# Optimization experiments

Measured on AMD Instinct MI355X. Metric: run time of the kernel, lower is better.

## Reference

```python
import jax, jax.numpy as jnp
import numpy as np

N_EMBD = 2048
N_HEAD = 32
N_KV_HEADS = 8
HEAD_DIM = 64
N_REP = N_HEAD // N_KV_HEADS
MAX_SEQ_LEN = 4096
ROPE_THETA = 10000.0


def _precompute_freqs_cis(dim, end, theta=ROPE_THETA):
    freqs = 1.0 / theta ** (jnp.arange(0, dim, 2)[: dim // 2].astype(jnp.float32) / dim)
    t = jnp.arange(end, dtype=jnp.float32)
    freqs = jnp.outer(t, freqs)  # (end, dim//2)
    return jnp.cos(freqs), jnp.sin(freqs)


def setup_inputs() -> dict:
    key = jax.random.key(0)
    ks = jax.random.split(key, 5)
    B, S = 2, 2048
    x = jax.random.normal(ks[0], (B, S, N_EMBD), dtype=jnp.float32)
    # torch Linear(in, out, bias=False): y = x @ W.T, W is (out, in). We store (in, out).
    sc = 1.0 / np.sqrt(N_EMBD)
    wq = jax.random.normal(ks[1], (N_EMBD, N_EMBD), dtype=jnp.float32) * sc
    wk = jax.random.normal(ks[2], (N_EMBD, N_KV_HEADS * HEAD_DIM), dtype=jnp.float32) * sc
    wv = jax.random.normal(ks[3], (N_EMBD, N_KV_HEADS * HEAD_DIM), dtype=jnp.float32) * sc
    wo = jax.random.normal(ks[4], (N_EMBD, N_EMBD), dtype=jnp.float32) * sc
    freqs_cos, freqs_sin = _precompute_freqs_cis(HEAD_DIM, MAX_SEQ_LEN)
    return {"x": x, "wq": wq, "wk": wk, "wv": wv, "wo": wo,
            "freqs_cos": freqs_cos, "freqs_sin": freqs_sin}


def _apply_rotary(t, cos, sin):
    # t: (B, S, H, HD); interleaved real/imag pairs along last dim.
    shp = t.shape
    t2 = t.reshape(*shp[:-1], HEAD_DIM // 2, 2)
    r, i = t2[..., 0], t2[..., 1]
    out_r = r * cos - i * sin
    out_i = r * sin + i * cos
    return jnp.stack([out_r, out_i], axis=-1).reshape(shp)


def reference(x, wq, wk, wv, wo, freqs_cos, freqs_sin):
    B, S, _ = x.shape
    xq = (x @ wq).reshape(B, S, N_HEAD, HEAD_DIM)
    xk = (x @ wk).reshape(B, S, N_KV_HEADS, HEAD_DIM)
    xv = (x @ wv).reshape(B, S, N_KV_HEADS, HEAD_DIM)

    cos = freqs_cos[:S][None, :, None, :]  # (1, S, 1, HD/2)
    sin = freqs_sin[:S][None, :, None, :]
    xq = _apply_rotary(xq, cos, sin)
    xk = _apply_rotary(xk, cos, sin)

    # GQA: repeat KV heads (repeat_interleave along head dim)
    keys = jnp.repeat(xk, N_REP, axis=2)    # (B, S, H, HD)
    values = jnp.repeat(xv, N_REP, axis=2)

    scores = jnp.einsum('bqhd,bkhd->bhqk', xq, keys) / np.sqrt(HEAD_DIM)
    causal = jnp.tril(jnp.ones((S, S), dtype=bool))
    scores = jnp.where(causal, scores, -jnp.inf)
    probs = jax.nn.softmax(scores.astype(jnp.float32), axis=-1).astype(xq.dtype)
    out = jnp.einsum('bhqk,bkhd->bqhd', probs, values)  # (B, S, H, HD)
    out = out.reshape(B, S, N_EMBD)
    return out @ wo
```

## Files before the change

kernel.cpp:

```cpp
#include <hip/hip_runtime.h>
#include <hip/hip_fp16.h>
#include <stdint.h>

typedef _Float16 f16x8 __attribute__((ext_vector_type(8)));
typedef _Float16 f16x4 __attribute__((ext_vector_type(4)));
typedef _Float16 f16x2 __attribute__((ext_vector_type(2)));
typedef float f32x4 __attribute__((ext_vector_type(4)));
typedef float f32x16 __attribute__((ext_vector_type(16)));

#define B_ 2
#define S_ 2048
#define NE 2048
#define NH 32
#define NKV 8
#define HD 64
#define NTOK (B_ * S_)
#define QKVN 3072

__device__ __forceinline__ f16x2 pk(float a, float b) {
  return __builtin_bit_cast(f16x2, __builtin_amdgcn_cvt_pkrtz(a, b));
}

__device__ __forceinline__ void gld_lds16(void* lds, const void* g) {
  __builtin_amdgcn_global_load_lds(
      (const __attribute__((address_space(1))) void*)g,
      (__attribute__((address_space(3))) void*)lds, 16, 0, 0);
}

#define PREP_CONV 16384
__global__ __launch_bounds__(256) void prep_kernel(
    const float* __restrict__ x, _Float16* __restrict__ xb,
    const float* __restrict__ wq, const float* __restrict__ wk,
    const float* __restrict__ wv, const float* __restrict__ wo,
    _Float16* __restrict__ wqkv_t, _Float16* __restrict__ wo_t) {
  const int bid = blockIdx.x;
  const int tid = threadIdx.x;
  if (bid < PREP_CONV) {
    int i = bid * 256 + tid;
    float2 v = ((const float2*)x)[i];
    f16x2 h;
    h.x = (_Float16)v.x;
    h.y = (_Float16)v.y;
    ((f16x2*)xb)[i] = h;
    return;
  }
  __shared__ float tile[32][33];
  int r = bid - PREP_CONV;
  const float* src;
  _Float16* dst;
  int srcN, rowoff, bx, by;
  if (r < 4096) {
    src = wq; dst = wqkv_t; srcN = 2048; rowoff = 0;
    bx = r & 63; by = r >> 6;
  } else if (r < 5120) {
    r -= 4096;
    src = wk; dst = wqkv_t; srcN = 512; rowoff = 2048;
    bx = r & 15; by = r >> 4;
  } else if (r < 6144) {
    r -= 5120;
    src = wv; dst = wqkv_t; srcN = 512; rowoff = 2560;
    bx = r & 15; by = r >> 4;
  } else {
    r -= 6144;
    src = wo; dst = wo_t; srcN = 2048; rowoff = 0;
    bx = r & 63; by = r >> 6;
  }
  const int n0 = bx * 32, k0 = by * 32;
  const int tx = tid & 31, ty = tid >> 5;
  for (int i = ty; i < 32; i += 8)
    tile[i][tx] = src[(size_t)(k0 + i) * srcN + n0 + tx];
  __syncthreads();
  for (int i = ty; i < 32; i += 8)
    dst[(size_t)(rowoff + n0 + i) * 2048 + k0 + tx] = (_Float16)tile[tx][i];
}

template <int OUT_F32>
__global__ __launch_bounds__(256, 2) void gemm_bt(
    const _Float16* __restrict__ A, const _Float16* __restrict__ Bt,
    void* __restrict__ Cout, int M, int N, int K) {
  __shared__ _Float16 As[128 * 32];
  __shared__ _Float16 Bs[128 * 32];
  const int tid = threadIdx.x;
  const int wave = tid >> 6, lane = tid & 63;
  const int qd = lane >> 4, ln = lane & 15;
  const int m0 = blockIdx.y * 128, n0 = blockIdx.x * 128;
  const int wm = (wave >> 1) * 64, wn = (wave & 1) * 64;

  f32x4 acc[4][4] = {};

  const int srow = (lane >> 2);
  const int scol = (lane & 3) * 8;

  for (int k0 = 0; k0 < K; k0 += 32) {
    __syncthreads();
#pragma unroll
    for (int it = 0; it < 2; ++it) {
      int r = wave * 32 + it * 16 + srow;
      gld_lds16(&As[(wave * 32 + it * 16) * 32],
                A + (size_t)(m0 + r) * K + k0 + scol);
      gld_lds16(&Bs[(wave * 32 + it * 16) * 32],
                Bt + (size_t)(n0 + r) * K + k0 + scol);
    }
    __syncthreads();
    f16x8 a[4], b[4];
#pragma unroll
    for (int mt = 0; mt < 4; ++mt)
      a[mt] = *(const f16x8*)&As[(wm + mt * 16 + ln) * 32 + qd * 8];
#pragma unroll
    for (int nt = 0; nt < 4; ++nt)
      b[nt] = *(const f16x8*)&Bs[(wn + nt * 16 + ln) * 32 + qd * 8];
#pragma unroll
    for (int mt = 0; mt < 4; ++mt)
#pragma unroll
      for (int nt = 0; nt < 4; ++nt)
        acc[mt][nt] =
            __builtin_amdgcn_mfma_f32_16x16x32_f16(a[mt], b[nt], acc[mt][nt], 0, 0, 0);
  }

#pragma unroll
  for (int mt = 0; mt < 4; ++mt) {
    int row = m0 + wm + mt * 16 + qd * 4;
#pragma unroll
    for (int nt = 0; nt < 4; ++nt) {
      int col = n0 + wn + nt * 16 + ln;
#pragma unroll
      for (int r = 0; r < 4; ++r) {
        if (OUT_F32)
          ((float*)Cout)[(size_t)(row + r) * N + col] = acc[mt][nt][r];
        else
          ((_Float16*)Cout)[(size_t)(row + r) * N + col] =
              (_Float16)acc[mt][nt][r];
      }
    }
  }
}

#define ROPE_BLKS 20480
__global__ __launch_bounds__(256) void rope_vtrans_kernel(
    const _Float16* __restrict__ qkv, const float* __restrict__ fcos,
    const float* __restrict__ fsin, _Float16* __restrict__ Qb,
    _Float16* __restrict__ Kb, _Float16* __restrict__ Vtg) {
  const int tid = threadIdx.x;
  if (blockIdx.x < ROPE_BLKS) {
    const float QSC = 0.125f * 1.44269504088896f;
    int idx = blockIdx.x * 256 + tid;
    int t = idx / 1280;
    int col = (idx - t * 1280) * 2;
    int b = t >> 11, s = t & 2047;
    float v0 = (float)qkv[(size_t)t * QKVN + col];
    float v1 = (float)qkv[(size_t)t * QKVN + col + 1];
    _Float16* dst;
    size_t off;
    int d;
    float sc;
    if (col < 2048) {
      int h = col >> 6;
      d = col & 63;
      dst = Qb;
      off = ((size_t)(b * NH + h) * S_ + s) * HD + d;
      sc = QSC;
    } else {
      int cc = col - 2048;
      int h = cc >> 6;
      d = cc & 63;
      dst = Kb;
      off = ((size_t)(b * NKV + h) * S_ + s) * HD + d;
      sc = 1.0f;
    }
    float c = fcos[s * 32 + (d >> 1)], sn = fsin[s * 32 + (d >> 1)];
    f16x2 o;
    o.x = (_Float16)((v0 * c - v1 * sn) * sc);
    o.y = (_Float16)((v0 * sn + v1 * c) * sc);
    *(f16x2*)(dst + off) = o;
    return;
  }
  __shared__ _Float16 tile[64][65];
  int r = blockIdx.x - ROPE_BLKS;
  int t0 = (r & 31) * 64;
  int kv = (r >> 5) & 7, b = r >> 8;
  for (int slot = tid; slot < 4096; slot += 256) {
    int rr = slot >> 6, c = slot & 63;
    tile[rr][c] = qkv[(size_t)(b * S_ + t0 + rr) * QKVN + 2560 + kv * 64 + c];
  }
  __syncthreads();
  size_t base = ((size_t)(b * NKV + kv) * HD) * S_;
  for (int slot = tid; slot < 4096; slot += 256) {
    int d = slot >> 6, rr = slot & 63;
    Vtg[base + (size_t)d * S_ + t0 + rr] = tile[rr][d];
  }
}

__global__ __launch_bounds__(128, 2) void attn_kernel(
    const _Float16* __restrict__ Qb, const _Float16* __restrict__ Kb,
    const _Float16* __restrict__ Vtg, _Float16* __restrict__ Ob) {
  constexpr float M_SHIFT = 10.0f;
  __shared__ _Float16 Ks[64 * 64];
  __shared__ _Float16 Vs[64 * 64];
  const int tid = threadIdx.x;
  const int wave = tid >> 6, lane = tid & 63;
  const int mrow = lane & 31;
  const bool half = (lane >> 5) != 0;
  const int h = blockIdx.y, b = blockIdx.z;
  const int kvh = h >> 2;

  const _Float16* Qh = Qb + ((size_t)(b * NH + h) * S_) * HD;
  const _Float16* Kh = Kb + ((size_t)(b * NKV + kvh) * S_) * HD;
  const _Float16* Vh = Vtg + ((size_t)(b * NKV + kvh) * HD) * S_;

  const int sr = tid >> 3;
  const int scc = tid & 7;
  const int swz = (scc ^ (sr & 7)) * 8;

#pragma unroll
  for (int pass = 0; pass < 2; ++pass) {
    const int qt = pass ? blockIdx.x : (31 - blockIdx.x);
    const int q0 = qt * 64;
    const int nkt = qt + 1;

    const int qrow = q0 + wave * 32 + mrow;
    f16x8 aq[4];
#pragma unroll
    for (int kk = 0; kk < 4; ++kk)
      aq[kk] = *(const f16x8*)(Qh + (size_t)qrow * HD + kk * 16 +
                               (half ? 8 : 0));

    f32x16 accO[2] = {};
    float lsum = 0.f;

    f16x8 kp[4], vp[4];
#pragma unroll
    for (int i = 0; i < 4; ++i) {
      kp[i] = *(const f16x8*)(Kh + (size_t)(sr + i * 16) * HD + scc * 8);
      vp[i] = *(const f16x8*)(Vh + (size_t)(sr + i * 16) * S_ + scc * 8);
    }
#pragma unroll
    for (int i = 0; i < 4; ++i) {
      *(f16x8*)&Ks[(sr + i * 16) * 64 + swz] = kp[i];
      *(f16x8*)&Vs[(sr + i * 16) * 64 + swz] = vp[i];
    }

    for (int kt = 0; kt < nkt; ++kt) {
      __syncthreads();
      if (kt + 1 < nkt) {
#pragma unroll
        for (int i = 0; i < 4; ++i) {
          kp[i] = *(const f16x8*)(Kh +
                                  (size_t)((kt + 1) * 64 + sr + i * 16) * HD +
                                  scc * 8);
          vp[i] = *(const f16x8*)(Vh + (size_t)(sr + i * 16) * S_ +
                                  (kt + 1) * 64 + scc * 8);
        }
      }

      f32x16 s[2];
#pragma unroll
      for (int nt = 0; nt < 2; ++nt)
#pragma unroll
        for (int r = 0; r < 16; ++r) s[nt][r] = -M_SHIFT;
#pragma unroll
      for (int kk = 0; kk < 4; ++kk) {
        int c = kk * 2 + (half ? 1 : 0);
#pragma unroll
        for (int nt = 0; nt < 2; ++nt) {
          int krow = nt * 32 + mrow;
          f16x8 bk = *(const f16x8*)&Ks[krow * 64 + ((c ^ (krow & 7)) * 8)];
          s[nt] = __builtin_amdgcn_mfma_f32_32x32x16_f16(bk, aq[kk], s[nt],
                                                         0, 0, 0);
        }
      }

      const bool edge = (kt == nkt - 1);
      float pf[2][16];
#pragma unroll
      for (int nt = 0; nt < 2; ++nt)
#pragma unroll
        for (int r = 0; r < 16; ++r) {
          int key = kt * 64 + nt * 32 + (r & 3) + 8 * (r >> 2) +
                    (half ? 4 : 0);
          float p = exp2f(s[nt][r]);
          if (edge && key > qrow) p = 0.f;
          lsum += p;
          pf[nt][r] = p;
        }

      f16x2 P2[2][4][2];
#pragma unroll
      for (int nt = 0; nt < 2; ++nt)
#pragma unroll
        for (int c = 0; c < 4; ++c)
#pragma unroll
          for (int u = 0; u < 2; ++u)
            P2[nt][c][u] = pk(pf[nt][4 * c + 2 * u], pf[nt][4 * c + 2 * u + 1]);

#pragma unroll
      for (int s4 = 0; s4 < 4; ++s4) {
        const int ntp = s4 >> 1;
        const int gA = (2 * s4) & 3, gB = (2 * s4 + 1) & 3;
        f16x2 own0 = half ? P2[ntp][gB][0] : P2[ntp][gA][0];
        f16x2 own1 = half ? P2[ntp][gB][1] : P2[ntp][gA][1];
        f16x2 snd0 = half ? P2[ntp][gA][0] : P2[ntp][gB][0];
        f16x2 snd1 = half ? P2[ntp][gA][1] : P2[ntp][gB][1];
        f16x2 rcv0 = __builtin_bit_cast(
            f16x2, __shfl_xor(__builtin_bit_cast(int, snd0), 32));
        f16x2 rcv1 = __builtin_bit_cast(
            f16x2, __shfl_xor(__builtin_bit_cast(int, snd1), 32));
        union {
          f16x2 h2[4];
          f16x8 h8;
        } bp;
        bp.h2[0] = half ? rcv0 : own0;
        bp.h2[1] = half ? rcv1 : own1;
        bp.h2[2] = half ? own0 : rcv0;
        bp.h2[3] = half ? own1 : rcv1;
        const int c = 2 * s4 + (half ? 1 : 0);
#pragma unroll
        for (int ntd = 0; ntd < 2; ++ntd) {
          int drow = ntd * 32 + mrow;
          f16x8 bv = *(const f16x8*)&Vs[drow * 64 + ((c ^ (drow & 7)) * 8)];
          accO[ntd] = __builtin_amdgcn_mfma_f32_32x32x16_f16(bv, bp.h8,
                                                             accO[ntd], 0, 0, 0);
        }
      }

      __syncthreads();
      if (kt + 1 < nkt) {
#pragma unroll
        for (int i = 0; i < 4; ++i) {
          *(f16x8*)&Ks[(sr + i * 16) * 64 + swz] = kp[i];
          *(f16x8*)&Vs[(sr + i * 16) * 64 + swz] = vp[i];
        }
      }
    }

    float tot = lsum + __shfl_xor(lsum, 32);
    float inv = 1.f / tot;
    size_t base = ((size_t)(b * S_) + qrow) * NE + h * HD;
#pragma unroll
    for (int ntd = 0; ntd < 2; ++ntd)
#pragma unroll
      for (int rq = 0; rq < 4; ++rq) {
        int d0 = ntd * 32 + 8 * rq + (half ? 4 : 0);
        union {
          f16x2 h2[2];
          f16x4 h4;
        } o;
        o.h2[0] = pk(accO[ntd][4 * rq + 0] * inv, accO[ntd][4 * rq + 1] * inv);
        o.h2[1] = pk(accO[ntd][4 * rq + 2] * inv, accO[ntd][4 * rq + 3] * inv);
        *(f16x4*)(Ob + base + d0) = o.h4;
      }
  }
}

extern "C" void kernel_launch(void* const* d_in, const int* in_sizes, int n_in,
                              void* d_out, int out_size, void* d_ws,
                              size_t ws_size, hipStream_t stream) {
  const float* x = (const float*)d_in[0];
  const float* wq = (const float*)d_in[1];
  const float* wk = (const float*)d_in[2];
  const float* wv = (const float*)d_in[3];
  const float* wo = (const float*)d_in[4];
  const float* fcos = (const float*)d_in[5];
  const float* fsin = (const float*)d_in[6];

  char* ws = (char*)d_ws;
  _Float16* xb = (_Float16*)(ws);
  _Float16* wqkv_t = (_Float16*)(ws + 16777216);
  _Float16* wo_t = (_Float16*)(ws + 29360128);
  _Float16* qkv = (_Float16*)(ws + 37748736);
  _Float16* Qb = (_Float16*)(ws + 62914560);
  _Float16* Kb = (_Float16*)(ws + 79691776);
  _Float16* Vb = (_Float16*)(ws + 83886080);
  _Float16* Ob = (_Float16*)(ws + 88080384);

  prep_kernel<<<PREP_CONV + 10240, 256, 0, stream>>>(x, xb, wq, wk, wv, wo,
                                                     wqkv_t, wo_t);

  gemm_bt<0><<<dim3(QKVN / 128, NTOK / 128), 256, 0, stream>>>(
      xb, wqkv_t, qkv, NTOK, QKVN, NE);

  rope_vtrans_kernel<<<ROPE_BLKS + 512, 256, 0, stream>>>(qkv, fcos, fsin,
                                                          Qb, Kb, Vb);

  attn_kernel<<<dim3(16, NH, B_), 128, 0, stream>>>(Qb, Kb, Vb, Ob);

  gemm_bt<1><<<dim3(NE / 128, NTOK / 128), 256, 0, stream>>>(
      Ob, wo_t, d_out, NTOK, NE, NE);
}
```

Baseline: 320.6 us.

## Deepen GEMM K-tile to 64, add MFMA priority hints and split softmax sums

The GEMM now stages a 64-wide K slice per iteration instead of 32, which halves the number of barrier pairs and issues twice as many MFMAs between syncs, at the cost of doubled LDS per block. The attention kernel raises wave priority around its MFMA blocks with s_setprio. The causal mask check now runs only on the diagonal tile. The row sum is computed from the packed fp16 probabilities using fdot2 into two independent accumulators. Summing rounded fp16 values slightly changes the normalisation numerics, and the unpadded 64-wide LDS rows may cause bank conflicts on the fragment reads.

Result: slower. 331.2 us (+3.3%).

```diff
diff --git a/kernel.cpp b/kernel.cpp
--- a/kernel.cpp
+++ b/kernel.cpp
@@ -20,6 +20,17 @@
 __device__ __forceinline__ f16x2 pk(float a, float b) {
   return __builtin_bit_cast(f16x2, __builtin_amdgcn_cvt_pkrtz(a, b));
 }
+
+#if __has_builtin(__builtin_amdgcn_fdot2)
+#define HAVE_FDOT2 1
+typedef __fp16 h16x2 __attribute__((ext_vector_type(2)));
+__device__ __forceinline__ float sum2(f16x2 a, float acc) {
+  h16x2 one;
+  one[0] = (__fp16)1.f;
+  one[1] = (__fp16)1.f;
+  return __builtin_amdgcn_fdot2(__builtin_bit_cast(h16x2, a), one, acc, false);
+}
+#endif
 
 __device__ __forceinline__ void gld_lds16(void* lds, const void* g) {
   __builtin_amdgcn_global_load_lds(
@@ -78,8 +89,8 @@
 __global__ __launch_bounds__(256, 2) void gemm_bt(
     const _Float16* __restrict__ A, const _Float16* __restrict__ Bt,
     void* __restrict__ Cout, int M, int N, int K) {
-  __shared__ _Float16 As[128 * 32];
-  __shared__ _Float16 Bs[128 * 32];
+  __shared__ _Float16 As[128 * 64];
+  __shared__ _Float16 Bs[128 * 64];
   const int tid = threadIdx.x;
   const int wave = tid >> 6, lane = tid & 63;
   const int qd = lane >> 4, ln = lane & 15;
@@ -88,33 +99,38 @@
 
   f32x4 acc[4][4] = {};
 
-  const int srow = (lane >> 2);
-  const int scol = (lane & 3) * 8;
-
-  for (int k0 = 0; k0 < K; k0 += 32) {
+  const int srow = lane >> 3;
+  const int scol = (lane & 7) * 8;
+
+  for (int k0 = 0; k0 < K; k0 += 64) {
     __syncthreads();
 #pragma unroll
-    for (int it = 0; it < 2; ++it) {
-      int r = wave * 32 + it * 16 + srow;
-      gld_lds16(&As[(wave * 32 + it * 16) * 32],
-                A + (size_t)(m0 + r) * K + k0 + scol);
-      gld_lds16(&Bs[(wave * 32 + it * 16) * 32],
-                Bt + (size_t)(n0 + r) * K + k0 + scol);
+    for (int j = 0; j < 4; ++j) {
+      int rb = wave * 32 + j * 8;
+      gld_lds16(&As[rb * 64], A + (size_t)(m0 + rb + srow) * K + k0 + scol);
+      gld_lds16(&Bs[rb * 64], Bt + (size_t)(n0 + rb + srow) * K + k0 + scol);
     }
     __syncthreads();
-    f16x8 a[4], b[4];
-#pragma unroll
-    for (int mt = 0; mt < 4; ++mt)
-      a[mt] = *(const f16x8*)&As[(wm + mt * 16 + ln) * 32 + qd * 8];
-#pragma unroll
-    for (int nt = 0; nt < 4; ++nt)
-      b[nt] = *(const f16x8*)&Bs[(wn + nt * 16 + ln) * 32 + qd * 8];
-#pragma unroll
-    for (int mt = 0; mt < 4; ++mt)
+    f16x8 a[2][4], b[2][4];
+#pragma unroll
+    for (int kk = 0; kk < 2; ++kk) {
+#pragma unroll
+      for (int mt = 0; mt < 4; ++mt)
+        a[kk][mt] =
+            *(const f16x8*)&As[(wm + mt * 16 + ln) * 64 + kk * 32 + qd * 8];
 #pragma unroll
       for (int nt = 0; nt < 4; ++nt)
-        acc[mt][nt] =
-            __builtin_amdgcn_mfma_f32_16x16x32_f16(a[mt], b[nt], acc[mt][nt], 0, 0, 0);
+        b[kk][nt] =
+            *(const f16x8*)&Bs[(wn + nt * 16 + ln) * 64 + kk * 32 + qd * 8];
+    }
+#pragma unroll
+    for (int kk = 0; kk < 2; ++kk)
+#pragma unroll
+      for (int mt = 0; mt < 4; ++mt)
+#pragma unroll
+        for (int nt = 0; nt < 4; ++nt)
+          acc[mt][nt] = __builtin_amdgcn_mfma_f32_16x16x32_f16(
+              a[kk][mt], b[kk][nt], acc[mt][nt], 0, 0, 0);
   }
 
 #pragma unroll
@@ -225,7 +241,7 @@
                                (half ? 8 : 0));
 
     f32x16 accO[2] = {};
-    float lsum = 0.f;
+    float lsum0 = 0.f, lsum1 = 0.f;
 
     f16x8 kp[4], vp[4];
 #pragma unroll
@@ -257,6 +273,7 @@
       for (int nt = 0; nt < 2; ++nt)
 #pragma unroll
         for (int r = 0; r < 16; ++r) s[nt][r] = -M_SHIFT;
+      __builtin_amdgcn_s_setprio(1);
 #pragma unroll
       for (int kk = 0; kk < 4; ++kk) {
         int c = kk * 2 + (half ? 1 : 0);
@@ -268,29 +285,49 @@
                                                          0, 0, 0);
         }
       }
+      __builtin_amdgcn_s_setprio(0);
 
       const bool edge = (kt == nkt - 1);
       float pf[2][16];
+      if (edge) {
+#pragma unroll
+        for (int nt = 0; nt < 2; ++nt)
+#pragma unroll
+          for (int r = 0; r < 16; ++r) {
+            int key = kt * 64 + nt * 32 + (r & 3) + 8 * (r >> 2) +
+                      (half ? 4 : 0);
+            float p = exp2f(s[nt][r]);
+            if (key > qrow) p = 0.f;
+            pf[nt][r] = p;
+          }
+      } else {
+#pragma unroll
+        for (int nt = 0; nt < 2; ++nt)
+#pragma unroll
+          for (int r = 0; r < 16; ++r) pf[nt][r] = exp2f(s[nt][r]);
+      }
+
+      f16x2 P2[2][4][2];
 #pragma unroll
       for (int nt = 0; nt < 2; ++nt)
 #pragma unroll
-        for (int r = 0; r < 16; ++r) {
-          int key = kt * 64 + nt * 32 + (r & 3) + 8 * (r >> 2) +
-                    (half ? 4 : 0);
-          float p = exp2f(s[nt][r]);
-          if (edge && key > qrow) p = 0.f;
-          lsum += p;
-          pf[nt][r] = p;
-        }
-
-      f16x2 P2[2][4][2];
-#pragma unroll
-      for (int nt = 0; nt < 2; ++nt)
-#pragma unroll
         for (int c = 0; c < 4; ++c)
 #pragma unroll
-          for (int u = 0; u < 2; ++u)
-            P2[nt][c][u] = pk(pf[nt][4 * c + 2 * u], pf[nt][4 * c + 2 * u + 1]);
+          for (int u = 0; u < 2; ++u) {
+            f16x2 v = pk(pf[nt][4 * c + 2 * u], pf[nt][4 * c + 2 * u + 1]);
+            P2[nt][c][u] = v;
+#ifdef HAVE_FDOT2
+            if (u == 0)
+              lsum0 = sum2(v, lsum0);
+            else
+              lsum1 = sum2(v, lsum1);
+#else
+            if (u == 0)
+              lsum0 += pf[nt][4 * c] + pf[nt][4 * c + 1];
+            else
+              lsum1 += pf[nt][4 * c + 2] + pf[nt][4 * c + 3];
+#endif
+          }
 
 #pragma unroll
       for (int s4 = 0; s4 < 4; ++s4) {
@@ -313,6 +350,7 @@
         bp.h2[2] = half ? own0 : rcv0;
         bp.h2[3] = half ? own1 : rcv1;
         const int c = 2 * s4 + (half ? 1 : 0);
+        __builtin_amdgcn_s_setprio(1);
 #pragma unroll
         for (int ntd = 0; ntd < 2; ++ntd) {
           int drow = ntd * 32 + mrow;
@@ -320,6 +358,7 @@
           accO[ntd] = __builtin_amdgcn_mfma_f32_32x32x16_f16(bv, bp.h8,
                                                              accO[ntd], 0, 0, 0);
         }
+        __builtin_amdgcn_s_setprio(0);
       }
 
       __syncthreads();
@@ -332,6 +371,7 @@
       }
     }
 
+    float lsum = lsum0 + lsum1;
     float tot = lsum + __shfl_xor(lsum, 32);
     float inv = 1.f / tot;
     size_t base = ((size_t)(b * S_) + qrow) * NE + h * HD;
```
